# Optimization experiments

Measured on AMD Instinct MI355X. Metric: run time of the kernel, lower is better.

## Reference

```python
import jax, jax.numpy as jnp
import numpy as np

CAP = 6.0
EPS = 1e-5

def _layernorm(x, g, b):
    mu = jnp.mean(x, axis=-1, keepdims=True)
    var = jnp.mean(jnp.square(x - mu), axis=-1, keepdims=True)
    return (x - mu) * jax.lax.rsqrt(var + EPS) * g + b

def setup_inputs() -> dict:
    key = jax.random.key(0)
    B, S, D, H = 4, 1024, 1024, 16
    DF = int(D * 2.0)
    ks = jax.random.split(key, 8)
    inp = {
        "x": jax.random.normal(ks[0], (B, S, D), dtype=jnp.float32),
        "mask": jnp.tril(jnp.ones((S, S), dtype=bool)),  # causal block mask
        "qkv_w": jax.random.normal(ks[1], (3 * D, D), dtype=jnp.float32) * 0.02,
        "qkv_b": jnp.zeros((3 * D,), dtype=jnp.float32),
        "out_w": jax.random.normal(ks[2], (D, D), dtype=jnp.float32) * 0.02,
        "out_b": jnp.zeros((D,), dtype=jnp.float32),
        "ln1_g": jnp.ones((D,), dtype=jnp.float32),
        "ln1_b": jnp.zeros((D,), dtype=jnp.float32),
        "ln2_g": jnp.ones((D,), dtype=jnp.float32),
        "ln2_b": jnp.zeros((D,), dtype=jnp.float32),
        "ff1_w": jax.random.normal(ks[3], (DF, D), dtype=jnp.float32) * 0.02,
        "ff1_b": jnp.zeros((DF,), dtype=jnp.float32),
        "ff2_w": jax.random.normal(ks[4], (D, DF), dtype=jnp.float32) * 0.02,
        "ff2_b": jnp.zeros((D,), dtype=jnp.float32),
    }
    return inp

def reference(x, mask, qkv_w, qkv_b, out_w, out_b, ln1_g, ln1_b, ln2_g, ln2_b,
              ff1_w, ff1_b, ff2_w, ff2_b):
    B, S, D = x.shape
    H = 16
    dh = D // H
    res = x
    h = _layernorm(x, ln1_g, ln1_b)
    qkv = h @ qkv_w.T + qkv_b                       # [B,S,3D]
    qkv = qkv.reshape(B, S, 3, H, dh).transpose(2, 0, 3, 1, 4)  # [3,B,H,S,dh]
    q, k, v = qkv[0], qkv[1], qkv[2]
    scores = jnp.einsum('bhqd,bhkd->bhqk', q, k) / jnp.sqrt(jnp.float32(dh))
    scores = CAP * jnp.tanh(scores / CAP)            # logit soft-cap score_mod
    scores = jnp.where(mask, scores, jnp.float32(-1e9))
    attn = jax.nn.softmax(scores, axis=-1)
    o = jnp.einsum('bhqk,bhkd->bhqd', attn, v)       # [B,H,S,dh]
    o = o.transpose(0, 2, 1, 3).reshape(B, S, D)
    x = res + (o @ out_w.T + out_b)
    h2 = _layernorm(x, ln2_g, ln2_b)
    ff = jax.nn.gelu(h2 @ ff1_w.T + ff1_b, approximate=False) @ ff2_w.T + ff2_b
    return x + ff
```

## Files before the change

kernel.cpp:

```cpp
#include <hip/hip_runtime.h>
#include <hip/hip_bf16.h>
#include <cmath>

#define NROWS 4096
#define DM    1024

typedef unsigned short u16;
typedef __attribute__((ext_vector_type(8))) short short8;
typedef __attribute__((ext_vector_type(4))) float floatx4;

#if __has_builtin(__builtin_amdgcn_exp2f)
#define EXP2F(x) __builtin_amdgcn_exp2f(x)
#else
#define EXP2F(x) exp2f(x)
#endif
#if __has_builtin(__builtin_amdgcn_rcpf)
#define RCPF(x) __builtin_amdgcn_rcpf(x)
#else
#define RCPF(x) (1.0f / (x))
#endif

__device__ __forceinline__ u16 f2bf(float f) {
    unsigned int u = __float_as_uint(f);
    return (u16)((u + 0x7fffu + ((u >> 16) & 1u)) >> 16);
}

__device__ __forceinline__ void gl_lds16(const u16* g, u16* l) {
    __builtin_amdgcn_global_load_lds(
        (const __attribute__((address_space(1))) unsigned int*)g,
        (__attribute__((address_space(3))) unsigned int*)l, 16, 0, 0);
}

__device__ __forceinline__ size_t pk_off(int row, int k, int KB) {
    const int rt = row >> 6, i = (row >> 4) & 3, lr = row & 15;
    const int kb = k >> 6, s = (k >> 5) & 1, lq = (k >> 3) & 3, j = k & 7;
    return ((((size_t)(rt * KB + kb) * 2 + s) * 4 + i) * 64 + lq * 16 + lr) * 8 + j;
}

__global__ __launch_bounds__(256) void castln_kernel(
    const float* __restrict__ s0, const float* __restrict__ s1,
    const float* __restrict__ s2, const float* __restrict__ s3,
    u16* __restrict__ d0, u16* __restrict__ d1,
    u16* __restrict__ d2, u16* __restrict__ d3,
    const float* __restrict__ x, const float* __restrict__ g,
    const float* __restrict__ beta, u16* __restrict__ hout)
{
    const int bid = blockIdx.x;
    if (bid < 8192) {
        const float* s; u16* d; int base, kbits, KB;
        if (bid < 3072)      { s = s0; d = d0; base = bid;        kbits = 10; KB = 16; }
        else if (bid < 4096) { s = s1; d = d1; base = bid - 3072; kbits = 10; KB = 16; }
        else if (bid < 6144) { s = s2; d = d2; base = bid - 4096; kbits = 10; KB = 16; }
        else                 { s = s3; d = d3; base = bid - 6144; kbits = 11; KB = 32; }
        const int idx = (base * 256 + threadIdx.x) * 4;
        const float4 v = *(const float4*)(s + idx);
        const int row = idx >> kbits, k = idx & ((1 << kbits) - 1);
        *(ushort4*)(d + pk_off(row, k, KB)) =
            make_ushort4(f2bf(v.x), f2bf(v.y), f2bf(v.z), f2bf(v.w));
        return;
    }
    const int row = bid - 8192;
    const int t = threadIdx.x;
    const float4 v = ((const float4*)(x + (size_t)row * DM))[t];
    float s = v.x + v.y + v.z + v.w;
    #pragma unroll
    for (int off = 32; off > 0; off >>= 1) s += __shfl_xor(s, off);
    __shared__ float red[4];
    const int wid = t >> 6;
    if ((t & 63) == 0) red[wid] = s;
    __syncthreads();
    const float mean = (red[0] + red[1] + red[2] + red[3]) * (1.0f / DM);
    const float dx = v.x - mean, dy = v.y - mean, dz = v.z - mean, dw = v.w - mean;
    float ss = dx*dx + dy*dy + dz*dz + dw*dw;
    #pragma unroll
    for (int off = 32; off > 0; off >>= 1) ss += __shfl_xor(ss, off);
    __syncthreads();
    if ((t & 63) == 0) red[wid] = ss;
    __syncthreads();
    const float var = (red[0] + red[1] + red[2] + red[3]) * (1.0f / DM);
    const float rstd = rsqrtf(var + 1e-5f);
    const float4 gv = ((const float4*)g)[t];
    const float4 bv = ((const float4*)beta)[t];
    *(ushort4*)(hout + pk_off(row, t * 4, 16)) = make_ushort4(
        f2bf(dx * rstd * gv.x + bv.x), f2bf(dy * rstd * gv.y + bv.y),
        f2bf(dz * rstd * gv.z + bv.z), f2bf(dw * rstd * gv.w + bv.w));
}

__global__ __launch_bounds__(256) void ln_kernel(
    const float* __restrict__ x, const float* __restrict__ g,
    const float* __restrict__ beta, u16* __restrict__ out)
{
    const int row = blockIdx.x;
    const int t = threadIdx.x;
    const float4 v = ((const float4*)(x + (size_t)row * DM))[t];
    float s = v.x + v.y + v.z + v.w;
    #pragma unroll
    for (int off = 32; off > 0; off >>= 1) s += __shfl_xor(s, off);
    __shared__ float red[4];
    const int wid = t >> 6;
    if ((t & 63) == 0) red[wid] = s;
    __syncthreads();
    const float mean = (red[0] + red[1] + red[2] + red[3]) * (1.0f / DM);
    const float dx = v.x - mean, dy = v.y - mean, dz = v.z - mean, dw = v.w - mean;
    float ss = dx*dx + dy*dy + dz*dz + dw*dw;
    #pragma unroll
    for (int off = 32; off > 0; off >>= 1) ss += __shfl_xor(ss, off);
    __syncthreads();
    if ((t & 63) == 0) red[wid] = ss;
    __syncthreads();
    const float var = (red[0] + red[1] + red[2] + red[3]) * (1.0f / DM);
    const float rstd = rsqrtf(var + 1e-5f);
    const float4 gv = ((const float4*)g)[t];
    const float4 bv = ((const float4*)beta)[t];
    *(ushort4*)(out + pk_off(row, t * 4, 16)) = make_ushort4(
        f2bf(dx * rstd * gv.x + bv.x), f2bf(dy * rstd * gv.y + bv.y),
        f2bf(dz * rstd * gv.z + bv.z), f2bf(dw * rstd * gv.w + bv.w));
}

__device__ __forceinline__ float gelu_f(float v) {
    return 0.5f * v * (1.0f + erff(v * 0.70710678118654752f));
}

template <int ACT, int OUTMODE, int TM>
__global__ __launch_bounds__(256, TM == 128 ? 3 : 2) void gemm_pk_kernel(
    const u16* __restrict__ A, const u16* __restrict__ W,
    const float* __restrict__ bias, const float* __restrict__ res,
    void* __restrict__ Cout, u16* __restrict__ vpout, u16* __restrict__ kpout,
    int N, int K)
{
    constexpr int MI = TM / 32;
    constexpr int NCH = (TM == 128) ? 4 : 3;
    constexpr int PHE = (TM == 128) ? 8192 : 12288;
    constexpr int TBUFB = 3 * PHE * 2;
    constexpr int EPIB = (OUTMODE == 1) ? 34816 : 17408;
    constexpr int SMEMB = (TBUFB > EPIB) ? TBUFB : EPIB;
    __shared__ __align__(16) char smem[SMEMB];
    u16* St = (u16*)smem;
    float* Cs = (float*)smem;

    const int tid = threadIdx.x;
    const int w = tid >> 6, l = tid & 63;
    const int lr = l & 15, lq = l >> 4;
    const int wm = w >> 1, wn = w & 1;

    const int fid = blockIdx.x;
    const int NB = (N >> 7) >> 3;
    const int xcd = fid & 7;
    const int kk = fid >> 3;
    constexpr int MT_BITS = (TM == 128) ? 5 : 6;
    constexpr int MT_MASK = (1 << MT_BITS) - 1;
    const int nt = xcd * NB + (kk >> MT_BITS);
    const int mt = kk & MT_MASK;
    const int m0 = mt * TM, n0 = nt * 128;
    const int KB = K >> 6;

    const u16* gch[NCH];
    if (TM == 128) {
        gch[0] = A + (size_t)(mt * 2 + 0) * KB * 4096;
        gch[1] = A + (size_t)(mt * 2 + 1) * KB * 4096;
        gch[2] = W + (size_t)(nt * 2 + 0) * KB * 4096;
        gch[3] = W + (size_t)(nt * 2 + 1) * KB * 4096;
    } else {
        gch[0] = A + (size_t)mt * KB * 4096;
        gch[1] = W + (size_t)(nt * 2 + 0) * KB * 4096;
        gch[2] = W + (size_t)(nt * 2 + 1) * KB * 4096;
    }

    floatx4 acc[MI][4] = {};

    auto STAGE = [&](int p, int buf) {
        if (TM == 128) {
            const int kb = p >> 1, s = p & 1;
            #pragma unroll
            for (int c = 0; c < NCH; c++)
                gl_lds16(gch[c] + (size_t)kb * 4096 + s * 2048 + w * 512 + l * 8,
                         St + buf * PHE + c * 2048 + w * 512);
        } else {
            #pragma unroll
            for (int c = 0; c < NCH; c++) {
                const u16* src = gch[c] + (size_t)p * 4096 + w * 512 + l * 8;
                u16* dst = St + buf * PHE + c * 4096 + w * 512;
                gl_lds16(src, dst);
                gl_lds16(src + 2048, dst + 2048);
            }
        }
    };

    auto COMPUTE = [&](int buf) {
        const u16* Sb = St + buf * PHE;
        if (TM == 128) {
            short8 af[4], bf[4];
            #pragma unroll
            for (int i = 0; i < 4; i++)
                af[i] = *(const short8*)(Sb + wm * 2048 + i * 512 + l * 8);
            #pragma unroll
            for (int j = 0; j < 4; j++)
                bf[j] = *(const short8*)(Sb + (2 + wn) * 2048 + j * 512 + l * 8);
            __builtin_amdgcn_s_setprio(1);
            #pragma unroll
            for (int i = 0; i < 4; i++)
                #pragma unroll
                for (int j = 0; j < 4; j++)
                    acc[i][j] = __builtin_amdgcn_mfma_f32_16x16x32_bf16(af[i], bf[j], acc[i][j], 0, 0, 0);
            __builtin_amdgcn_s_setprio(0);
        } else {
            #pragma unroll
            for (int ts = 0; ts < 2; ts++) {
                short8 af[2], bf[4];
                #pragma unroll
                for (int i = 0; i < 2; i++)
                    af[i] = *(const short8*)(Sb + ts * 2048 + (wm * 2 + i) * 512 + l * 8);
                #pragma unroll
                for (int j = 0; j < 4; j++)
                    bf[j] = *(const short8*)(Sb + (1 + wn) * 4096 + ts * 2048 + j * 512 + l * 8);
                __builtin_amdgcn_s_setprio(1);
                #pragma unroll
                for (int i = 0; i < 2; i++)
                    #pragma unroll
                    for (int j = 0; j < 4; j++)
                        acc[i][j] = __builtin_amdgcn_mfma_f32_16x16x32_bf16(af[i], bf[j], acc[i][j], 0, 0, 0);
                __builtin_amdgcn_s_setprio(0);
            }
        }
    };

    const int NPH = (TM == 128) ? (K >> 5) : (K >> 6);
    STAGE(0, 0);
    STAGE(1, 1);
    int bcur = 0;
    for (int p = 0; p < NPH; p++) {
        if (p + 2 < NPH) {
            STAGE(p + 2, (p + 2) % 3);
            if (TM == 128) asm volatile("s_waitcnt vmcnt(8)" ::: "memory");
            else           asm volatile("s_waitcnt vmcnt(12)" ::: "memory");
        } else if (p + 1 < NPH) {
            if (TM == 128) asm volatile("s_waitcnt vmcnt(4)" ::: "memory");
            else           asm volatile("s_waitcnt vmcnt(6)" ::: "memory");
        } else {
            asm volatile("s_waitcnt vmcnt(0)" ::: "memory");
        }
        __builtin_amdgcn_s_barrier();
        __builtin_amdgcn_sched_barrier(0);
        COMPUTE(bcur);
        __builtin_amdgcn_s_barrier();
        bcur = (bcur + 1) % 3;
    }

    if (OUTMODE == 1) {
        short* Ts = (short*)smem;
        float bj[4];
        #pragma unroll
        for (int j = 0; j < 4; j++) bj[j] = bias[n0 + wn * 64 + j * 16 + lr];
        const bool isV = (n0 >= 2048);
        if (isV) {
            #pragma unroll
            for (int i = 0; i < 4; i++)
                #pragma unroll
                for (int j = 0; j < 4; j++) {
                    const int vcol_l = wn * 64 + j * 16 + lr;
                    const int sbase = wm * 64 + i * 16 + lq * 4;
                    #pragma unroll
                    for (int rp = 0; rp < 2; rp++) {
                        const unsigned pkv =
                            (unsigned)f2bf(acc[i][j][rp * 2] + bj[j]) |
                            ((unsigned)f2bf(acc[i][j][rp * 2 + 1] + bj[j]) << 16);
                        *(unsigned*)&Ts[vcol_l * 136 + sbase + rp * 2] = pkv;
                    }
                }
        } else {
            #pragma unroll
            for (int i = 0; i < 4; i++)
                #pragma unroll
                for (int j = 0; j < 4; j++)
                    #pragma unroll
                    for (int r = 0; r < 4; r++) {
                        const int row_l = wm * 64 + i * 16 + lq * 4 + r;
                        const int col_l = wn * 64 + j * 16 + lr;
                        Ts[row_l * 136 + col_l] = (short)f2bf(acc[i][j][r] + bj[j]);
                    }
        }
        __syncthreads();
        u16* dbuf = isV ? vpout : (n0 >= 1024 ? kpout : (u16*)Cout);
        const int hbase = (n0 & 1023) >> 6;
        const int l0 = (tid * 2) & 63, subp = tid >> 6, sp = (tid >> 5) & 1;
        #pragma unroll
        for (int tl = 0; tl < 2; tl++) {
            const int mg = m0 + tl * 64;
            const int bb2 = mg >> 10, ktile = (mg & 1023) >> 6;
            #pragma unroll
            for (int hl = 0; hl < 2; hl++) {
                const int hh = hbase + hl;
                u16* dst = dbuf + ((size_t)(bb2 * 16 + hh) * 16 + ktile) * 4096 + tid * 16;
                #pragma unroll
                for (int half = 0; half < 2; half++) {
                    const int ll = l0 + half;
                    short8 seg;
                    if (isV) {
                        const int vcol_l = hl * 64 + subp * 16 + (ll & 15);
                        const int srow = tl * 64 + sp * 32 + ((ll >> 4) & 3) * 8;
                        seg = *(const short8*)&Ts[vcol_l * 136 + srow];
                    } else {
                        const int row_l = tl * 64 + subp * 16 + (ll & 15);
                        const int col_l = hl * 64 + sp * 32 + ((ll >> 4) & 3) * 8;
                        seg = *(const short8*)&Ts[row_l * 136 + col_l];
                    }
                    *(short8*)(dst + half * 8) = seg;
                }
            }
        }
        return;
    }

    #pragma unroll
    for (int i = 0; i < MI; i++) {
        __syncthreads();
        #pragma unroll
        for (int r = 0; r < 4; r++) {
            const int rl = wm * 16 + lq * 4 + r;
            #pragma unroll
            for (int j = 0; j < 4; j++)
                Cs[rl * 136 + wn * 64 + j * 16 + lr] = acc[i][j][r];
        }
        __syncthreads();
        #pragma unroll
        for (int q = 0; q < 2; q++) {
            const int s2 = tid * 2 + q;
            const int rid = s2 >> 4, c8 = s2 & 15;
            const int rr = m0 + (rid >> 4) * (TM / 2) + i * 16 + (rid & 15);
            const int col = c8 * 8;
            float vv[8];
            const float4 v0 = *(const float4*)&Cs[rid * 136 + col];
            const float4 v1 = *(const float4*)&Cs[rid * 136 + col + 4];
            const float4 ba = *(const float4*)&bias[n0 + col];
            const float4 bb4 = *(const float4*)&bias[n0 + col + 4];
            vv[0] = v0.x + ba.x;  vv[1] = v0.y + ba.y;  vv[2] = v0.z + ba.z;  vv[3] = v0.w + ba.w;
            vv[4] = v1.x + bb4.x; vv[5] = v1.y + bb4.y; vv[6] = v1.z + bb4.z; vv[7] = v1.w + bb4.w;
            if (ACT) {
                #pragma unroll
                for (int e = 0; e < 8; e++) vv[e] = gelu_f(vv[e]);
            }
            if (OUTMODE == 0) {
                const size_t o0 = (size_t)rr * N + n0 + col;
                if (res) {
                    const float4 r0 = *(const float4*)&res[o0];
                    const float4 r1 = *(const float4*)&res[o0 + 4];
                    vv[0]+=r0.x; vv[1]+=r0.y; vv[2]+=r0.z; vv[3]+=r0.w;
                    vv[4]+=r1.x; vv[5]+=r1.y; vv[6]+=r1.z; vv[7]+=r1.w;
                }
                *(float4*)((float*)Cout + o0)     = make_float4(vv[0], vv[1], vv[2], vv[3]);
                *(float4*)((float*)Cout + o0 + 4) = make_float4(vv[4], vv[5], vv[6], vv[7]);
            } else {
                short8 ov;
                #pragma unroll
                for (int e = 0; e < 8; e++) ov[e] = (short)f2bf(vv[e]);
                *(short8*)((u16*)Cout + pk_off(rr, n0 + col, N >> 6)) = ov;
            }
        }
    }
}

__global__ __launch_bounds__(256, 3) void attn_mfma_kernel(
    const u16* __restrict__ qp, const u16* __restrict__ kp,
    const u16* __restrict__ vp, u16* __restrict__ o)
{
    __shared__ __align__(16) short Ps[4][1152];
    __shared__ __align__(16) short Os[4096];
    __shared__ __align__(16) u16 Kl[2][4096];
    __shared__ __align__(16) u16 Vl[2][4096];

    const int qt = 15 - blockIdx.y;
    const int bh = blockIdx.x;
    const int b = bh >> 4, h = bh & 15;
    const int tid = threadIdx.x;
    const int w = tid >> 6, l = tid & 63;
    const int C = l & 15, Qd = l >> 4;

    const float C1f = 0.0601122935f, C2f = -17.3123404907f;

    const size_t headoff = (size_t)(b * 16 + h) * 16 * 4096;
    const u16* qb = qp + headoff + (size_t)qt * 4096 + w * 1024 + l * 8;
    const u16* kb = kp + headoff;
    const u16* vb = vp + headoff;

    short8 qf[2];
    qf[0] = *(const short8*)qb;
    qf[1] = *(const short8*)(qb + 512);

    float l_i = 0.f;
    floatx4 oacc[4] = {};

    auto STAGEKV = [&](int kt, int buf) {
        const u16* ks = kb + (size_t)kt * 4096 + (w * 2) * 512 + l * 8;
        const u16* vs = vb + (size_t)kt * 4096 + (w * 2) * 512 + l * 8;
        u16* kd = &Kl[buf][(w * 2) * 512];
        u16* vd = &Vl[buf][(w * 2) * 512];
        gl_lds16(ks, kd);
        gl_lds16(ks + 512, kd + 512);
        gl_lds16(vs, vd);
        gl_lds16(vs + 512, vd + 512);
    };

    int cur = 0;
    STAGEKV(0, 0);
    __syncthreads();

    for (int kt = 0; kt <= qt; kt++) {
        if (kt < qt) STAGEKV(kt + 1, cur ^ 1);

        const u16* Kc = &Kl[cur][0];
        const u16* Vc = &Vl[cur][0];
        short8 kf[8];
        #pragma unroll
        for (int i = 0; i < 8; i++) kf[i] = *(const short8*)(Kc + i * 512 + l * 8);

        floatx4 sacc[4] = {};
        __builtin_amdgcn_s_setprio(1);
        #pragma unroll
        for (int mt = 0; mt < 4; mt++)
            #pragma unroll
            for (int s = 0; s < 2; s++)
                sacc[mt] = __builtin_amdgcn_mfma_f32_16x16x32_bf16(kf[mt * 2 + s], qf[s], sacc[mt], 0, 0, 0);
        __builtin_amdgcn_s_setprio(0);

        float p[16];
        float rs = 0.f;
        const bool diag = (kt == qt);
        const int qrow = qt * 64 + w * 16 + C;
        #pragma unroll
        for (int mt = 0; mt < 4; mt++)
            #pragma unroll
            for (int r = 0; r < 4; r++) {
                const float e = EXP2F(sacc[mt][r] * C1f);
                float pv = EXP2F(C2f * RCPF(e + 1.0f));
                if (diag) {
                    const int krow = kt * 64 + mt * 16 + Qd * 4 + r;
                    if (krow > qrow) pv = 0.f;
                }
                p[mt * 4 + r] = pv;
                rs += pv;
            }
        rs += __shfl_xor(rs, 16);
        rs += __shfl_xor(rs, 32);
        l_i += rs;

        #pragma unroll
        for (int mt = 0; mt < 4; mt++)
            #pragma unroll
            for (int pr = 0; pr < 2; pr++) {
                union { __hip_bfloat162 b2; unsigned u; } cv;
                cv.b2 = __float22bfloat162_rn(
                    make_float2(p[mt * 4 + pr * 2], p[mt * 4 + pr * 2 + 1]));
                *(unsigned*)&Ps[w][C * 72 + mt * 16 + Qd * 4 + pr * 2] = cv.u;
            }
        short8 pf[2];
        pf[0] = *(const short8*)&Ps[w][C * 72 + Qd * 8];
        pf[1] = *(const short8*)&Ps[w][C * 72 + 32 + Qd * 8];

        short8 vf[8];
        #pragma unroll
        for (int j = 0; j < 8; j++) vf[j] = *(const short8*)(Vc + j * 512 + l * 8);

        __builtin_amdgcn_s_setprio(1);
        #pragma unroll
        for (int dt = 0; dt < 4; dt++)
            #pragma unroll
            for (int s = 0; s < 2; s++)
                oacc[dt] = __builtin_amdgcn_mfma_f32_16x16x32_bf16(pf[s], vf[dt * 2 + s], oacc[dt], 0, 0, 0);
        __builtin_amdgcn_s_setprio(0);

        __syncthreads();
        cur ^= 1;
    }

    float linv[4];
    #pragma unroll
    for (int r = 0; r < 4; r++) linv[r] = RCPF(__shfl(l_i, Qd * 4 + r));
    #pragma unroll
    for (int dt = 0; dt < 4; dt++) {
        const int s = dt >> 1;
        const int lqp = (dt & 1) * 2 + (C >> 3);
        const int jj = C & 7;
        #pragma unroll
        for (int r = 0; r < 4; r++)
            Os[((s * 4 + w) * 64 + lqp * 16 + Qd * 4 + r) * 8 + jj] =
                (short)f2bf(oacc[dt][r] * linv[r]);
    }
    __syncthreads();
    u16* obase = o + (size_t)((b * 16 + qt) * 16 + h) * 4096 + tid * 16;
    *(short8*)obase       = *(const short8*)&Os[tid * 16];
    *(short8*)(obase + 8) = *(const short8*)&Os[tid * 16 + 8];
}

extern "C" void kernel_launch(void* const* d_in, const int* in_sizes, int n_in,
                              void* d_out, int out_size, void* d_ws, size_t ws_size,
                              hipStream_t stream)
{
    (void)in_sizes; (void)n_in; (void)out_size; (void)ws_size;
    const float* x     = (const float*)d_in[0];
    const float* qkv_w = (const float*)d_in[2];
    const float* qkv_b = (const float*)d_in[3];
    const float* out_w = (const float*)d_in[4];
    const float* out_b = (const float*)d_in[5];
    const float* ln1_g = (const float*)d_in[6];
    const float* ln1_b = (const float*)d_in[7];
    const float* ln2_g = (const float*)d_in[8];
    const float* ln2_b = (const float*)d_in[9];
    const float* ff1_w = (const float*)d_in[10];
    const float* ff1_b = (const float*)d_in[11];
    const float* ff2_w = (const float*)d_in[12];
    const float* ff2_b = (const float*)d_in[13];
    float* out = (float*)d_out;

    u16* qpbuf = (u16*)d_ws;
    u16* kpbuf = qpbuf + 4194304;
    u16* vpbuf = kpbuf + 4194304;
    u16* hbuf  = (u16*)((char*)d_ws + 33554432);
    u16* obuf  = (u16*)((char*)d_ws + 41943040);
    u16* wq    = (u16*)((char*)d_ws + 50331648);
    u16* wo = wq + 3145728;
    u16* w1 = wo + 1048576;
    u16* w2 = w1 + 2097152;
    u16* ff1buf = (u16*)d_ws;

    castln_kernel<<<12288, 256, 0, stream>>>(
        qkv_w, out_w, ff1_w, ff2_w, wq, wo, w1, w2, x, ln1_g, ln1_b, hbuf);
    gemm_pk_kernel<0,1,128><<<768, 256, 0, stream>>>(
        hbuf, wq, qkv_b, nullptr, qpbuf, vpbuf, kpbuf, 3072, 1024);
    attn_mfma_kernel<<<dim3(64, 16), 256, 0, stream>>>(qpbuf, kpbuf, vpbuf, obuf);
    gemm_pk_kernel<0,0,64><<<512, 256, 0, stream>>>(
        obuf, wo, out_b, x, out, nullptr, nullptr, 1024, 1024);
    ln_kernel<<<NROWS, 256, 0, stream>>>(out, ln2_g, ln2_b, hbuf);
    gemm_pk_kernel<1,2,128><<<512, 256, 0, stream>>>(
        hbuf, w1, ff1_b, nullptr, ff1buf, nullptr, nullptr, 2048, 1024);
    gemm_pk_kernel<0,0,64><<<512, 256, 0, stream>>>(
        ff1buf, w2, ff2_b, out, out, nullptr, nullptr, 1024, 2048);
}
```

Before: 268.2 us.

## Move out/ff1/ff2 weight casts into attention kernel grid to overlap

The fp32-to-bf16 packing of the out, ff1 and ff2 weights moves out of the first cast+layernorm kernel and into extra blocks appended to the attention kernel's grid. The attention grid is flattened to 1D, with the first 1024 blocks doing attention and the rest doing casts. The aim is to shorten the critical path before the QKV GEMM and let the memory-bound cast blocks fill idle CUs during the compute-bound, causally imbalanced attention. The cast blocks are scheduled after the attention blocks and still use the attention kernel's LDS and occupancy limits, so they may just run at the tail.

```diff
diff --git a/kernel.cpp b/kernel.cpp
--- a/kernel.cpp
+++ b/kernel.cpp
@@ -38,28 +38,20 @@
 }
 
 __global__ __launch_bounds__(256) void castln_kernel(
-    const float* __restrict__ s0, const float* __restrict__ s1,
-    const float* __restrict__ s2, const float* __restrict__ s3,
-    u16* __restrict__ d0, u16* __restrict__ d1,
-    u16* __restrict__ d2, u16* __restrict__ d3,
+    const float* __restrict__ s0, u16* __restrict__ d0,
     const float* __restrict__ x, const float* __restrict__ g,
     const float* __restrict__ beta, u16* __restrict__ hout)
 {
     const int bid = blockIdx.x;
-    if (bid < 8192) {
-        const float* s; u16* d; int base, kbits, KB;
-        if (bid < 3072)      { s = s0; d = d0; base = bid;        kbits = 10; KB = 16; }
-        else if (bid < 4096) { s = s1; d = d1; base = bid - 3072; kbits = 10; KB = 16; }
-        else if (bid < 6144) { s = s2; d = d2; base = bid - 4096; kbits = 10; KB = 16; }
-        else                 { s = s3; d = d3; base = bid - 6144; kbits = 11; KB = 32; }
-        const int idx = (base * 256 + threadIdx.x) * 4;
-        const float4 v = *(const float4*)(s + idx);
-        const int row = idx >> kbits, k = idx & ((1 << kbits) - 1);
-        *(ushort4*)(d + pk_off(row, k, KB)) =
+    if (bid < 3072) {
+        const int idx = (bid * 256 + threadIdx.x) * 4;
+        const float4 v = *(const float4*)(s0 + idx);
+        const int row = idx >> 10, k = idx & 1023;
+        *(ushort4*)(d0 + pk_off(row, k, 16)) =
             make_ushort4(f2bf(v.x), f2bf(v.y), f2bf(v.z), f2bf(v.w));
         return;
     }
-    const int row = bid - 8192;
+    const int row = bid - 3072;
     const int t = threadIdx.x;
     const float4 v = ((const float4*)(x + (size_t)row * DM))[t];
     float s = v.x + v.y + v.z + v.w;
@@ -361,15 +353,33 @@
 
 __global__ __launch_bounds__(256, 3) void attn_mfma_kernel(
     const u16* __restrict__ qp, const u16* __restrict__ kp,
-    const u16* __restrict__ vp, u16* __restrict__ o)
+    const u16* __restrict__ vp, u16* __restrict__ o,
+    const float* __restrict__ cs0, const float* __restrict__ cs1,
+    const float* __restrict__ cs2, u16* __restrict__ cd0,
+    u16* __restrict__ cd1, u16* __restrict__ cd2)
 {
+    const int bid = blockIdx.x;
+    if (bid >= 1024) {
+        const int cbid = bid - 1024;
+        const float* s; u16* d; int base, kbits, KB;
+        if (cbid < 1024)      { s = cs0; d = cd0; base = cbid;        kbits = 10; KB = 16; }
+        else if (cbid < 3072) { s = cs1; d = cd1; base = cbid - 1024; kbits = 10; KB = 16; }
+        else                  { s = cs2; d = cd2; base = cbid - 3072; kbits = 11; KB = 32; }
+        const int idx = (base * 256 + threadIdx.x) * 4;
+        const float4 v = *(const float4*)(s + idx);
+        const int row = idx >> kbits, k = idx & ((1 << kbits) - 1);
+        *(ushort4*)(d + pk_off(row, k, KB)) =
+            make_ushort4(f2bf(v.x), f2bf(v.y), f2bf(v.z), f2bf(v.w));
+        return;
+    }
+
     __shared__ __align__(16) short Ps[4][1152];
     __shared__ __align__(16) short Os[4096];
     __shared__ __align__(16) u16 Kl[2][4096];
     __shared__ __align__(16) u16 Vl[2][4096];
 
-    const int qt = 15 - blockIdx.y;
-    const int bh = blockIdx.x;
+    const int qt = 15 - (bid >> 6);
+    const int bh = bid & 63;
     const int b = bh >> 4, h = bh & 15;
     const int tid = threadIdx.x;
     const int w = tid >> 6, l = tid & 63;
@@ -522,11 +532,12 @@
     u16* w2 = w1 + 2097152;
     u16* ff1buf = (u16*)d_ws;
 
-    castln_kernel<<<12288, 256, 0, stream>>>(
-        qkv_w, out_w, ff1_w, ff2_w, wq, wo, w1, w2, x, ln1_g, ln1_b, hbuf);
+    castln_kernel<<<7168, 256, 0, stream>>>(
+        qkv_w, wq, x, ln1_g, ln1_b, hbuf);
     gemm_pk_kernel<0,1,128><<<768, 256, 0, stream>>>(
         hbuf, wq, qkv_b, nullptr, qpbuf, vpbuf, kpbuf, 3072, 1024);
-    attn_mfma_kernel<<<dim3(64, 16), 256, 0, stream>>>(qpbuf, kpbuf, vpbuf, obuf);
+    attn_mfma_kernel<<<6144, 256, 0, stream>>>(
+        qpbuf, kpbuf, vpbuf, obuf, out_w, ff1_w, ff2_w, wo, w1, w2);
     gemm_pk_kernel<0,0,64><<<512, 256, 0, stream>>>(
         obuf, wo, out_b, x, out, nullptr, nullptr, 1024, 1024);
     ln_kernel<<<NROWS, 256, 0, stream>>>(out, ln2_g, ln2_b, hbuf);
```

Result: no change. 273.1 us (+1.9%).

## Single-buffer V and alias output staging to cut attention LDS for occupancy

Applied to the files above, without the earlier changes.

The attention kernel now keeps K double-buffered but stages V into a single buffer loaded within the same iteration, and reuses the K buffer for the output staging tile. The goal is to reduce LDS per block so four blocks fit per CU instead of three. Synchronisation changes from __syncthreads to explicit vmcnt waits plus s_barrier at two points per iteration. V loads are now exposed within the iteration rather than prefetched a tile ahead, and the hand-counted vmcnt values must match the number of issued loads exactly.

```diff
diff --git a/kernel.cpp b/kernel.cpp
--- a/kernel.cpp
+++ b/kernel.cpp
@@ -359,14 +359,13 @@
     }
 }
 
-__global__ __launch_bounds__(256, 3) void attn_mfma_kernel(
+__global__ __launch_bounds__(256, 4) void attn_mfma_kernel(
     const u16* __restrict__ qp, const u16* __restrict__ kp,
     const u16* __restrict__ vp, u16* __restrict__ o)
 {
     __shared__ __align__(16) short Ps[4][1152];
-    __shared__ __align__(16) short Os[4096];
     __shared__ __align__(16) u16 Kl[2][4096];
-    __shared__ __align__(16) u16 Vl[2][4096];
+    __shared__ __align__(16) u16 Vl[4096];
 
     const int qt = 15 - blockIdx.y;
     const int bh = blockIdx.x;
@@ -389,26 +388,33 @@
     float l_i = 0.f;
     floatx4 oacc[4] = {};
 
-    auto STAGEKV = [&](int kt, int buf) {
-        const u16* ks = kb + (size_t)kt * 4096 + (w * 2) * 512 + l * 8;
-        const u16* vs = vb + (size_t)kt * 4096 + (w * 2) * 512 + l * 8;
-        u16* kd = &Kl[buf][(w * 2) * 512];
-        u16* vd = &Vl[buf][(w * 2) * 512];
+    auto STAGEK = [&](int kt, int buf) {
+        const u16* ks = kb + (size_t)kt * 4096 + w * 1024 + l * 8;
+        u16* kd = &Kl[buf][w * 1024];
         gl_lds16(ks, kd);
         gl_lds16(ks + 512, kd + 512);
+    };
+    auto STAGEV = [&](int kt) {
+        const u16* vs = vb + (size_t)kt * 4096 + w * 1024 + l * 8;
+        u16* vd = &Vl[w * 1024];
         gl_lds16(vs, vd);
         gl_lds16(vs + 512, vd + 512);
     };
 
+    STAGEK(0, 0);
     int cur = 0;
-    STAGEKV(0, 0);
-    __syncthreads();
 
     for (int kt = 0; kt <= qt; kt++) {
-        if (kt < qt) STAGEKV(kt + 1, cur ^ 1);
+        const bool more = (kt < qt);
+        STAGEV(kt);
+        if (more) STAGEK(kt + 1, cur ^ 1);
+
+        if (more) asm volatile("s_waitcnt vmcnt(4)" ::: "memory");
+        else      asm volatile("s_waitcnt vmcnt(2)" ::: "memory");
+        __builtin_amdgcn_s_barrier();
+        __builtin_amdgcn_sched_barrier(0);
 
         const u16* Kc = &Kl[cur][0];
-        const u16* Vc = &Vl[cur][0];
         short8 kf[8];
         #pragma unroll
         for (int i = 0; i < 8; i++) kf[i] = *(const short8*)(Kc + i * 512 + l * 8);
@@ -456,9 +462,14 @@
         pf[0] = *(const short8*)&Ps[w][C * 72 + Qd * 8];
         pf[1] = *(const short8*)&Ps[w][C * 72 + 32 + Qd * 8];
 
+        if (more) asm volatile("s_waitcnt vmcnt(2)" ::: "memory");
+        else      asm volatile("s_waitcnt vmcnt(0)" ::: "memory");
+        __builtin_amdgcn_s_barrier();
+        __builtin_amdgcn_sched_barrier(0);
+
         short8 vf[8];
         #pragma unroll
-        for (int j = 0; j < 8; j++) vf[j] = *(const short8*)(Vc + j * 512 + l * 8);
+        for (int j = 0; j < 8; j++) vf[j] = *(const short8*)(Vl + j * 512 + l * 8);
 
         __builtin_amdgcn_s_setprio(1);
         #pragma unroll
@@ -468,10 +479,11 @@
                 oacc[dt] = __builtin_amdgcn_mfma_f32_16x16x32_bf16(pf[s], vf[dt * 2 + s], oacc[dt], 0, 0, 0);
         __builtin_amdgcn_s_setprio(0);
 
-        __syncthreads();
+        __builtin_amdgcn_s_barrier();
         cur ^= 1;
     }
 
+    short* Os = (short*)&Kl[0][0];
     float linv[4];
     #pragma unroll
     for (int r = 0; r < 4; r++) linv[r] = RCPF(__shfl(l_i, Qd * 4 + r));
```

Measured after the change: 271.3 us. No clear change (+1.2%).
